# Kernel tuning notes

Measured on AMD Instinct MI355X. Metric: run time of the kernel, lower is better.

The kernel has to match this reference:

```python
import jax, jax.numpy as jnp
import numpy as np

N_HEADS = 16


def setup_inputs() -> dict:
    key = jax.random.key(0)
    k1, k2, k3, k4, k5 = jax.random.split(key, 5)
    B, S, D = 2, 2048, 1024
    return {
        "query": jax.random.normal(k1, (B, S, D), dtype=jnp.float32),
        "key": jax.random.normal(k2, (B, S, D), dtype=jnp.float32),
        "value": jax.random.normal(k3, (B, S, D), dtype=jnp.float32),
        "fc_w": jax.random.normal(k4, (D, D), dtype=jnp.float32) * (1.0 / np.sqrt(D)),
        "fc_b": jax.random.normal(k5, (D,), dtype=jnp.float32) * 0.01,
    }


def reference(query, key, value, fc_w, fc_b):
    b, s, d = query.shape
    head_dim = d // N_HEADS
    q = query.reshape(b, s, N_HEADS, head_dim)
    k = key.reshape(b, s, N_HEADS, head_dim)
    v = value.reshape(b, s, N_HEADS, head_dim)
    # energy: [b, n, q, k]
    energy = jnp.einsum('bqnd,bknd->bnqk', q, k)
    scale = 1.0 / jnp.sqrt(jnp.asarray(head_dim, dtype=energy.dtype))
    attn = jax.nn.softmax(energy * scale, axis=3)
    out = jnp.einsum('bnqk,bknd->bqnd', attn, v).reshape(b, s, d)
    # fc: y = x @ W^T + b (torch Linear convention)
    return out @ fc_w.T + fc_b
```

## Files before the change

kernel.cpp:

```cpp
#include <hip/hip_runtime.h>
#include <hip/hip_bf16.h>

#define BATCH 2
#define SEQ 2048
#define DMODEL 1024
#define NHEADS 16
#define HDIM 64
#define KVBLK 64
#define NCHUNK (SEQ / KVBLK)
#define NITER (NCHUNK / 2)

#define QSCALE 0.180336880f
#define DEFER_THR 8.0f

typedef __bf16 bf16x8 __attribute__((ext_vector_type(8)));
typedef __bf16 bf16x4 __attribute__((ext_vector_type(4)));
typedef float f32x4 __attribute__((ext_vector_type(4)));
typedef float f32x16 __attribute__((ext_vector_type(16)));
typedef unsigned int uint2v __attribute__((ext_vector_type(2)));

union B8u { unsigned int u[4]; bf16x8 v; };

__device__ __forceinline__ unsigned int cvt_pk_bf16(float lo, float hi) {
  unsigned int d;
  asm("v_cvt_pk_bf16_f32 %0, %1, %2" : "=v"(d) : "v"(lo), "v"(hi));
  return d;
}

__device__ __forceinline__ void permlane32_swap(unsigned &a, unsigned &b) {
  auto r = __builtin_amdgcn_permlane32_swap(a, b, false, false);
  unsigned tmp[2];
  __builtin_memcpy(tmp, &r, 8);
  a = tmp[0]; b = tmp[1];
}

__global__ __launch_bounds__(256)
void conv_all(const float* __restrict__ K, __bf16* __restrict__ Kbf,
              const float* __restrict__ V, __bf16* __restrict__ Vt,
              const float* __restrict__ W, __bf16* __restrict__ Wbf) {
  const int p = blockIdx.x;
  __shared__ __bf16 T[64][72];

  if (p < 2048) {
    const int t = p * 256 + threadIdx.x;
    const int d8 = t & 7, key = (t >> 3) & (SEQ - 1), g = t >> 14;
    const float* src = K + ((size_t)(g >> 4) * SEQ + key) * DMODEL +
                       (g & 15) * HDIM + d8 * 8;
    f32x4 a = *reinterpret_cast<const f32x4*>(src);
    f32x4 c = *reinterpret_cast<const f32x4*>(src + 4);
    bf16x8 o;
#pragma unroll
    for (int j = 0; j < 4; ++j) { o[j] = (__bf16)a[j]; o[4 + j] = (__bf16)c[j]; }
    *reinterpret_cast<bf16x8*>(Kbf + (size_t)t * 8) = o;
  } else if (p < 3072) {
    const int blk = p - 2048;
    const int g = blk >> 5, c0 = (blk & 31) * 64;
    const int b = g >> 4, h = g & 15;
    {
      const int key = threadIdx.x >> 2, dq = threadIdx.x & 3;
      const float* src = V + ((size_t)(b * SEQ) + c0 + key) * DMODEL +
                         h * HDIM + dq * 16;
#pragma unroll
      for (int i = 0; i < 4; ++i) {
        f32x4 v = *reinterpret_cast<const f32x4*>(src + 4 * i);
        bf16x4 o;
#pragma unroll
        for (int j = 0; j < 4; ++j) o[j] = (__bf16)v[j];
        *reinterpret_cast<bf16x4*>(&T[key][dq * 16 + 4 * i]) = o;
      }
    }
    __syncthreads();
    {
      const int d = threadIdx.x >> 2, kq = threadIdx.x & 3;
      bf16x8 r0, r1;
#pragma unroll
      for (int i = 0; i < 8; ++i) {
        r0[i] = T[kq * 16 + i][d];
        r1[i] = T[kq * 16 + 8 + i][d];
      }
      __bf16* dst = Vt + ((size_t)g * HDIM + d) * SEQ + c0 + kq * 16;
      *reinterpret_cast<bf16x8*>(dst) = r0;
      *reinterpret_cast<bf16x8*>(dst + 8) = r1;
    }
  } else {
    const int t = (p - 3072) * 256 + threadIdx.x;
    f32x4 a = *reinterpret_cast<const f32x4*>(W + (size_t)t * 8);
    f32x4 c = *reinterpret_cast<const f32x4*>(W + (size_t)t * 8 + 4);
    bf16x8 o;
#pragma unroll
    for (int j = 0; j < 4; ++j) { o[j] = (__bf16)a[j]; o[4 + j] = (__bf16)c[j]; }
    *reinterpret_cast<bf16x8*>(Wbf + (size_t)t * 8) = o;
  }
}

__global__ __launch_bounds__(512, 4)
void attn_kernel(const float* __restrict__ Q, const __bf16* __restrict__ Kbf,
                 const __bf16* __restrict__ Vt, __bf16* __restrict__ O) {
  const int p = blockIdx.x;
  const int xcd = p & 7, slot = p >> 3;
  const int g = xcd + 8 * (slot >> 4);
  const int b = g >> 4, h = g & 15;
  const int q0 = (slot & 15) * 128;

  const int tid = threadIdx.x;
  const int wave = tid >> 6, lane = tid & 63;
  const int qg = wave & 3, ks = wave >> 2;
  const int l31 = lane & 31, hi = lane >> 5;
  const int ob = hi << 4;
  const int swz = (l31 & 7) << 4;

  __shared__ __align__(16) __bf16 SM[2][2][64 * 64];
  __shared__ float mlb[2][4][32];

  const int qrow = q0 + (qg << 5) + l31;
  const float* qp = Q + ((size_t)(b * SEQ + qrow)) * DMODEL + h * HDIM;
  bf16x8 qf[4];
#pragma unroll
  for (int kd = 0; kd < 4; ++kd) {
    f32x4 a = *reinterpret_cast<const f32x4*>(qp + kd * 16 + hi * 8);
    f32x4 c = *reinterpret_cast<const f32x4*>(qp + kd * 16 + hi * 8 + 4);
#pragma unroll
    for (int j = 0; j < 4; ++j) {
      qf[kd][j]     = (__bf16)(a[j] * QSCALE);
      qf[kd][4 + j] = (__bf16)(c[j] * QSCALE);
    }
  }

  f32x16 oacc0, oacc1;
#pragma unroll
  for (int r = 0; r < 16; ++r) { oacc0[r] = 0.f; oacc1[r] = 0.f; }
  float m_run = -1e30f, l_run = 0.f;

  const __bf16* kgb = Kbf + (size_t)g * SEQ * HDIM;
  const __bf16* vgb = Vt + (size_t)g * HDIM * SEQ;

  const int t2 = tid & 255;
  const int sk_key = t2 >> 2, sk_dq = t2 & 3;
  const int sv_dim = t2 >> 2, sv_kq = t2 & 3;
  const int ksw = (sk_key & 7) << 4;
  const int vsw = (sv_dim & 7) << 4;

  bf16x8 kr0, kr1, vr0, vr1;

#define STAGE_LOAD(C0)                                                        \
  do {                                                                        \
    const __bf16* kc = kgb + (size_t)(C0 + sk_key) * HDIM + sk_dq * 16;       \
    kr0 = *reinterpret_cast<const bf16x8*>(kc);                               \
    kr1 = *reinterpret_cast<const bf16x8*>(kc + 8);                           \
    const __bf16* vc = vgb + (size_t)sv_dim * SEQ + (C0) + sv_kq * 16;        \
    vr0 = *reinterpret_cast<const bf16x8*>(vc);                               \
    vr1 = *reinterpret_cast<const bf16x8*>(vc + 8);                           \
  } while (0)

#define STAGE_WRITE()                                                         \
  do {                                                                        \
    char* kdst = (char*)(&SM[ks][0][0]) + sk_key * 128;                       \
    *reinterpret_cast<bf16x8*>(kdst + (((sk_dq << 5)) ^ ksw)) = kr0;          \
    *reinterpret_cast<bf16x8*>(kdst + (((sk_dq << 5) | 16) ^ ksw)) = kr1;     \
    char* vdst = (char*)(&SM[ks][1][0]) + sv_dim * 128;                       \
    *reinterpret_cast<bf16x8*>(vdst + (((sv_kq << 5)) ^ vsw)) = vr0;          \
    *reinterpret_cast<bf16x8*>(vdst + (((sv_kq << 5) | 16) ^ vsw)) = vr1;     \
  } while (0)

  STAGE_LOAD(ks * NITER * KVBLK);
  STAGE_WRITE();
  __syncthreads();
  STAGE_LOAD((ks * NITER + 1) * KVBLK);

  for (int i = 0; i < NITER; ++i) {
    const char* kb = (const char*)(&SM[ks][0][0]);
    const char* vb = (const char*)(&SM[ks][1][0]);

    f32x16 s0, s1;
#pragma unroll
    for (int r = 0; r < 16; ++r) { s0[r] = 0.f; s1[r] = 0.f; }
    __builtin_amdgcn_s_setprio(1);
#pragma unroll
    for (int kd = 0; kd < 4; ++kd) {
      bf16x8 a0 = *reinterpret_cast<const bf16x8*>(
          kb + l31 * 128 + (((kd << 5) | ob) ^ swz));
      bf16x8 a1 = *reinterpret_cast<const bf16x8*>(
          kb + (32 + l31) * 128 + (((kd << 5) | ob) ^ swz));
      s0 = __builtin_amdgcn_mfma_f32_32x32x16_bf16(a0, qf[kd], s0, 0, 0, 0);
      s1 = __builtin_amdgcn_mfma_f32_32x32x16_bf16(a1, qf[kd], s1, 0, 0, 0);
    }
    __builtin_amdgcn_s_setprio(0);

    float m8[8];
#pragma unroll
    for (int r = 0; r < 8; ++r)
      m8[r] = fmaxf(fmaxf(s0[r], s0[r + 8]), fmaxf(s1[r], s1[r + 8]));
    float pm = fmaxf(fmaxf(fmaxf(m8[0], m8[1]), fmaxf(m8[2], m8[3])),
                     fmaxf(fmaxf(m8[4], m8[5]), fmaxf(m8[6], m8[7])));
    pm = fmaxf(pm, __shfl_xor(pm, 32, 64));

    if (!__all(pm <= m_run + DEFER_THR)) {
      float mu = fmaxf(m_run, pm);
      float al = __builtin_amdgcn_exp2f(m_run - mu);
      m_run = mu;
      l_run *= al;
#pragma unroll
      for (int r = 0; r < 16; ++r) { oacc0[r] *= al; oacc1[r] *= al; }
    }

#pragma unroll
    for (int r = 0; r < 16; ++r) {
      s0[r] = __builtin_amdgcn_exp2f(s0[r] - m_run);
      s1[r] = __builtin_amdgcn_exp2f(s1[r] - m_run);
    }
    float t8[8];
#pragma unroll
    for (int r = 0; r < 8; ++r)
      t8[r] = (s0[r] + s0[r + 8]) + (s1[r] + s1[r + 8]);
    float ts = ((t8[0] + t8[1]) + (t8[2] + t8[3])) +
               ((t8[4] + t8[5]) + (t8[6] + t8[7]));
    ts += __shfl_xor(ts, 32, 64);
    l_run += ts;

    B8u pfr[4];
#pragma unroll
    for (int kq = 0; kq < 4; ++kq) {
      f32x16 ps = (kq < 2) ? s0 : s1;
      const int r0 = (kq & 1) * 8;
      unsigned lo0 = cvt_pk_bf16(ps[r0 + 0], ps[r0 + 1]);
      unsigned lo1 = cvt_pk_bf16(ps[r0 + 2], ps[r0 + 3]);
      unsigned h0  = cvt_pk_bf16(ps[r0 + 4], ps[r0 + 5]);
      unsigned h1  = cvt_pk_bf16(ps[r0 + 6], ps[r0 + 7]);
      permlane32_swap(lo0, h0);
      permlane32_swap(lo1, h1);
      pfr[kq].u[0] = lo0; pfr[kq].u[1] = lo1;
      pfr[kq].u[2] = h0;  pfr[kq].u[3] = h1;
    }

    __builtin_amdgcn_s_setprio(1);
#pragma unroll
    for (int kq = 0; kq < 4; ++kq) {
      bf16x8 v0 = *reinterpret_cast<const bf16x8*>(
          vb + l31 * 128 + (((kq << 5) | ob) ^ swz));
      bf16x8 v1 = *reinterpret_cast<const bf16x8*>(
          vb + (32 + l31) * 128 + (((kq << 5) | ob) ^ swz));
      oacc0 = __builtin_amdgcn_mfma_f32_32x32x16_bf16(v0, pfr[kq].v, oacc0, 0, 0, 0);
      oacc1 = __builtin_amdgcn_mfma_f32_32x32x16_bf16(v1, pfr[kq].v, oacc1, 0, 0, 0);
    }
    __builtin_amdgcn_s_setprio(0);

    __syncthreads();
    if (i + 1 < NITER) {
      STAGE_WRITE();
      if (i + 2 < NITER) STAGE_LOAD((ks * NITER + i + 2) * KVBLK);
    }
    __syncthreads();
  }

  float* Ob = (float*)&SM[0][0][0];

  if (ks == 1) {
    if (hi == 0) { mlb[0][qg][l31] = m_run; mlb[1][qg][l31] = l_run; }
#pragma unroll
    for (int dt = 0; dt < 2; ++dt) {
      f32x16 oa = dt ? oacc1 : oacc0;
#pragma unroll
      for (int r = 0; r < 16; ++r) {
        int dim = dt * 32 + (r & 3) + 8 * (r >> 2) + 4 * hi;
        Ob[(qg * 64 + dim) * 32 + l31] = oa[r];
      }
    }
  }
  __syncthreads();

  if (ks == 0) {
    float m1 = mlb[0][qg][l31], l1 = mlb[1][qg][l31];
    float m = fmaxf(m_run, m1);
    float a0 = __builtin_amdgcn_exp2f(m_run - m);
    float a1 = __builtin_amdgcn_exp2f(m1 - m);
    const float inv = 1.0f / (a0 * l_run + a1 * l1);
    __bf16* op = O + ((size_t)(b * SEQ + qrow)) * DMODEL + h * HDIM;
#pragma unroll
    for (int dt = 0; dt < 2; ++dt) {
      f32x16 oa = dt ? oacc1 : oacc0;
#pragma unroll
      for (int a = 0; a < 4; ++a) {
        float e[4];
#pragma unroll
        for (int j = 0; j < 4; ++j) {
          int r = 4 * a + j;
          int dim = dt * 32 + (r & 3) + 8 * (r >> 2) + 4 * hi;
          float opart = Ob[(qg * 64 + dim) * 32 + l31];
          e[j] = (oa[r] * a0 + opart * a1) * inv;
        }
        uint2v w;
        w[0] = cvt_pk_bf16(e[0], e[1]);
        w[1] = cvt_pk_bf16(e[2], e[3]);
        *reinterpret_cast<uint2v*>((char*)op + (dt * 32 + a * 8 + hi * 4) * 2) = w;
      }
    }
  }
#undef STAGE_LOAD
#undef STAGE_WRITE
}

__global__ __launch_bounds__(256)
void fc_kernel(const __bf16* __restrict__ X, const __bf16* __restrict__ W,
               const float* __restrict__ bias, float* __restrict__ Y) {
  const int p = blockIdx.x;
  const int xcd = p & 7, slot = p >> 3;
  const int m0 = (xcd + 8 * (slot >> 4)) * 128;
  const int n0 = (slot & 15) * 64;

  const int tid = threadIdx.x;
  const int wave = tid >> 6, lane = tid & 63;
  const int g = lane >> 4, lr = lane & 15;
  const int wm = wave >> 1, wn = wave & 1;

  __shared__ __bf16 As[128][72];
  __shared__ __bf16 Bs[64][72];

  f32x4 acc[4][2];
#pragma unroll
  for (int i = 0; i < 4; ++i)
#pragma unroll
    for (int j = 0; j < 2; ++j) acc[i][j] = (f32x4){0.f, 0.f, 0.f, 0.f};

  float bv[2];
#pragma unroll
  for (int j = 0; j < 2; ++j) bv[j] = bias[n0 + wn * 32 + 16 * j + lr];

  bf16x8 av[4], wv[2];

#define FC_LOAD(KK)                                                          \
  do {                                                                       \
    _Pragma("unroll") for (int e = 0; e < 4; ++e) {                          \
      int idx = tid + 256 * e;                                               \
      int row = idx >> 3, k8 = idx & 7;                                      \
      av[e] = *reinterpret_cast<const bf16x8*>(                              \
          X + (size_t)(m0 + row) * DMODEL + (KK) + k8 * 8);                  \
    }                                                                        \
    _Pragma("unroll") for (int e = 0; e < 2; ++e) {                          \
      int idx = tid + 256 * e;                                               \
      int row = idx >> 3, k8 = idx & 7;                                      \
      wv[e] = *reinterpret_cast<const bf16x8*>(                              \
          W + (size_t)(n0 + row) * DMODEL + (KK) + k8 * 8);                  \
    }                                                                        \
  } while (0)

#define FC_WRITE()                                                           \
  do {                                                                       \
    _Pragma("unroll") for (int e = 0; e < 4; ++e) {                          \
      int idx = tid + 256 * e;                                               \
      int row = idx >> 3, k8 = idx & 7;                                      \
      *reinterpret_cast<bf16x8*>(&As[row][k8 * 8]) = av[e];                  \
    }                                                                        \
    _Pragma("unroll") for (int e = 0; e < 2; ++e) {                          \
      int idx = tid + 256 * e;                                               \
      int row = idx >> 3, k8 = idx & 7;                                      \
      *reinterpret_cast<bf16x8*>(&Bs[row][k8 * 8]) = wv[e];                  \
    }                                                                        \
  } while (0)

  FC_LOAD(0);

  for (int kk = 0; kk < DMODEL; kk += 64) {
    __syncthreads();
    FC_WRITE();
    __syncthreads();
    if (kk + 64 < DMODEL) FC_LOAD(kk + 64);

#pragma unroll
    for (int ks2 = 0; ks2 < 2; ++ks2) {
      bf16x8 af[4], bfr[2];
#pragma unroll
      for (int i = 0; i < 4; ++i)
        af[i] = *reinterpret_cast<const bf16x8*>(
            &As[wm * 64 + 16 * i + lr][ks2 * 32 + g * 8]);
#pragma unroll
      for (int j = 0; j < 2; ++j)
        bfr[j] = *reinterpret_cast<const bf16x8*>(
            &Bs[wn * 32 + 16 * j + lr][ks2 * 32 + g * 8]);
#pragma unroll
      for (int i = 0; i < 4; ++i)
#pragma unroll
        for (int j = 0; j < 2; ++j)
          acc[i][j] = __builtin_amdgcn_mfma_f32_16x16x32_bf16(
              af[i], bfr[j], acc[i][j], 0, 0, 0);
    }
  }

#pragma unroll
  for (int i = 0; i < 4; ++i) {
    int m = m0 + wm * 64 + 16 * i + g * 4;
#pragma unroll
    for (int j = 0; j < 2; ++j) {
      int n = n0 + wn * 32 + 16 * j + lr;
      float* yp = Y + (size_t)m * DMODEL + n;
#pragma unroll
      for (int r = 0; r < 4; ++r) yp[(size_t)r * DMODEL] = acc[i][j][r] + bv[j];
    }
  }
#undef FC_LOAD
#undef FC_WRITE
}

extern "C" void kernel_launch(void* const* d_in, const int* in_sizes, int n_in,
                              void* d_out, int out_size, void* d_ws, size_t ws_size,
                              hipStream_t stream) {
  const float* q    = (const float*)d_in[0];
  const float* k    = (const float*)d_in[1];
  const float* v    = (const float*)d_in[2];
  const float* w    = (const float*)d_in[3];
  const float* bias = (const float*)d_in[4];
  float* out = (float*)d_out;

  char* ws = (char*)d_ws;
  __bf16* O   = (__bf16*)(ws);
  __bf16* Kbf = (__bf16*)(ws + (8u << 20));
  __bf16* Vt  = (__bf16*)(ws + (16u << 20));
  __bf16* Wbf = (__bf16*)(ws + (24u << 20));

  conv_all<<<dim3(3584), 256, 0, stream>>>(k, Kbf, v, Vt, w, Wbf);
  attn_kernel<<<dim3(512), 512, 0, stream>>>(q, Kbf, Vt, O);
  fc_kernel<<<dim3(512), 256, 0, stream>>>(O, Wbf, bias, out);
}
```

Before: 83.82 us.

## Split KV four ways per block with 64-row query tiles and tree combine

Each attention block now covers 64 query rows instead of 128, and its eight waves split the sequence into four KV partitions instead of two. The grid doubles to 1024 blocks and the KV chunk shrinks from 64 to 32 keys. The V tile drops its XOR swizzle for a padded row stride. Partial softmax states are merged in stages through shared memory, with three dump/combine rounds. The aim is better load balance and occupancy across CUs, at the cost of more barriers per key processed, smaller MFMA batches per iteration and extra combine work.

```diff
diff --git a/kernel.cpp b/kernel.cpp
--- a/kernel.cpp
+++ b/kernel.cpp
@@ -6,9 +6,9 @@
 #define DMODEL 1024
 #define NHEADS 16
 #define HDIM 64
-#define KVBLK 64
-#define NCHUNK (SEQ / KVBLK)
-#define NITER (NCHUNK / 2)
+#define NSPLIT 4
+#define KVB 32
+#define NIT (SEQ / NSPLIT / KVB)
 
 #define QSCALE 0.180336880f
 #define DEFER_THR 8.0f
@@ -98,19 +98,20 @@
                  const __bf16* __restrict__ Vt, __bf16* __restrict__ O) {
   const int p = blockIdx.x;
   const int xcd = p & 7, slot = p >> 3;
-  const int g = xcd + 8 * (slot >> 4);
+  const int g = xcd + 8 * (slot >> 5);
   const int b = g >> 4, h = g & 15;
-  const int q0 = (slot & 15) * 128;
+  const int q0 = (slot & 31) * 64;
 
   const int tid = threadIdx.x;
   const int wave = tid >> 6, lane = tid & 63;
-  const int qg = wave & 3, ks = wave >> 2;
+  const int qg = wave & 1, ks = wave >> 1;
   const int l31 = lane & 31, hi = lane >> 5;
   const int ob = hi << 4;
   const int swz = (l31 & 7) << 4;
 
-  __shared__ __align__(16) __bf16 SM[2][2][64 * 64];
-  __shared__ float mlb[2][4][32];
+  __shared__ __align__(16) __bf16 SK[4][32 * 64];
+  __shared__ __align__(16) __bf16 SV[4][64 * 40];
+  __shared__ float mlb[3][2][2][32];
 
   const int qrow = q0 + (qg << 5) + l31;
   const float* qp = Q + ((size_t)(b * SEQ + qrow)) * DMODEL + h * HDIM;
@@ -134,62 +135,57 @@
   const __bf16* kgb = Kbf + (size_t)g * SEQ * HDIM;
   const __bf16* vgb = Vt + (size_t)g * HDIM * SEQ;
 
-  const int t2 = tid & 255;
+  const int t2 = tid & 127;
   const int sk_key = t2 >> 2, sk_dq = t2 & 3;
-  const int sv_dim = t2 >> 2, sv_kq = t2 & 3;
+  const int sv_dim = t2 >> 1, sv_kh = t2 & 1;
   const int ksw = (sk_key & 7) << 4;
-  const int vsw = (sv_dim & 7) << 4;
 
   bf16x8 kr0, kr1, vr0, vr1;
 
 #define STAGE_LOAD(C0)                                                        \
   do {                                                                        \
-    const __bf16* kc = kgb + (size_t)(C0 + sk_key) * HDIM + sk_dq * 16;       \
+    const __bf16* kc = kgb + (size_t)((C0) + sk_key) * HDIM + sk_dq * 16;     \
     kr0 = *reinterpret_cast<const bf16x8*>(kc);                               \
     kr1 = *reinterpret_cast<const bf16x8*>(kc + 8);                           \
-    const __bf16* vc = vgb + (size_t)sv_dim * SEQ + (C0) + sv_kq * 16;        \
+    const __bf16* vc = vgb + (size_t)sv_dim * SEQ + (C0) + sv_kh * 16;        \
     vr0 = *reinterpret_cast<const bf16x8*>(vc);                               \
     vr1 = *reinterpret_cast<const bf16x8*>(vc + 8);                           \
   } while (0)
 
 #define STAGE_WRITE()                                                         \
   do {                                                                        \
-    char* kdst = (char*)(&SM[ks][0][0]) + sk_key * 128;                       \
+    char* kdst = (char*)(&SK[ks][0]) + sk_key * 128;                          \
     *reinterpret_cast<bf16x8*>(kdst + (((sk_dq << 5)) ^ ksw)) = kr0;          \
     *reinterpret_cast<bf16x8*>(kdst + (((sk_dq << 5) | 16) ^ ksw)) = kr1;     \
-    char* vdst = (char*)(&SM[ks][1][0]) + sv_dim * 128;                       \
-    *reinterpret_cast<bf16x8*>(vdst + (((sv_kq << 5)) ^ vsw)) = vr0;          \
-    *reinterpret_cast<bf16x8*>(vdst + (((sv_kq << 5) | 16) ^ vsw)) = vr1;     \
-  } while (0)
-
-  STAGE_LOAD(ks * NITER * KVBLK);
+    char* vdst = (char*)(&SV[ks][0]) + sv_dim * 80 + sv_kh * 32;              \
+    *reinterpret_cast<bf16x8*>(vdst) = vr0;                                   \
+    *reinterpret_cast<bf16x8*>(vdst + 16) = vr1;                              \
+  } while (0)
+
+  STAGE_LOAD(ks * 512);
   STAGE_WRITE();
   __syncthreads();
-  STAGE_LOAD((ks * NITER + 1) * KVBLK);
-
-  for (int i = 0; i < NITER; ++i) {
-    const char* kb = (const char*)(&SM[ks][0][0]);
-    const char* vb = (const char*)(&SM[ks][1][0]);
-
-    f32x16 s0, s1;
-#pragma unroll
-    for (int r = 0; r < 16; ++r) { s0[r] = 0.f; s1[r] = 0.f; }
+  STAGE_LOAD(ks * 512 + KVB);
+
+  for (int i = 0; i < NIT; ++i) {
+    const char* kb = (const char*)(&SK[ks][0]);
+    const char* vb = (const char*)(&SV[ks][0]);
+
+    f32x16 s;
+#pragma unroll
+    for (int r = 0; r < 16; ++r) s[r] = 0.f;
     __builtin_amdgcn_s_setprio(1);
 #pragma unroll
     for (int kd = 0; kd < 4; ++kd) {
       bf16x8 a0 = *reinterpret_cast<const bf16x8*>(
           kb + l31 * 128 + (((kd << 5) | ob) ^ swz));
-      bf16x8 a1 = *reinterpret_cast<const bf16x8*>(
-          kb + (32 + l31) * 128 + (((kd << 5) | ob) ^ swz));
-      s0 = __builtin_amdgcn_mfma_f32_32x32x16_bf16(a0, qf[kd], s0, 0, 0, 0);
-      s1 = __builtin_amdgcn_mfma_f32_32x32x16_bf16(a1, qf[kd], s1, 0, 0, 0);
+      s = __builtin_amdgcn_mfma_f32_32x32x16_bf16(a0, qf[kd], s, 0, 0, 0);
     }
     __builtin_amdgcn_s_setprio(0);
 
     float m8[8];
 #pragma unroll
-    for (int r = 0; r < 8; ++r)
-      m8[r] = fmaxf(fmaxf(s0[r], s0[r + 8]), fmaxf(s1[r], s1[r + 8]));
+    for (int r = 0; r < 8; ++r) m8[r] = fmaxf(s[r], s[r + 8]);
     float pm = fmaxf(fmaxf(fmaxf(m8[0], m8[1]), fmaxf(m8[2], m8[3])),
                      fmaxf(fmaxf(m8[4], m8[5]), fmaxf(m8[6], m8[7])));
     pm = fmaxf(pm, __shfl_xor(pm, 32, 64));
@@ -204,28 +200,23 @@
     }
 
 #pragma unroll
-    for (int r = 0; r < 16; ++r) {
-      s0[r] = __builtin_amdgcn_exp2f(s0[r] - m_run);
-      s1[r] = __builtin_amdgcn_exp2f(s1[r] - m_run);
-    }
+    for (int r = 0; r < 16; ++r) s[r] = __builtin_amdgcn_exp2f(s[r] - m_run);
     float t8[8];
 #pragma unroll
-    for (int r = 0; r < 8; ++r)
-      t8[r] = (s0[r] + s0[r + 8]) + (s1[r] + s1[r + 8]);
+    for (int r = 0; r < 8; ++r) t8[r] = s[r] + s[r + 8];
     float ts = ((t8[0] + t8[1]) + (t8[2] + t8[3])) +
                ((t8[4] + t8[5]) + (t8[6] + t8[7]));
     ts += __shfl_xor(ts, 32, 64);
     l_run += ts;
 
-    B8u pfr[4];
-#pragma unroll
-    for (int kq = 0; kq < 4; ++kq) {
-      f32x16 ps = (kq < 2) ? s0 : s1;
-      const int r0 = (kq & 1) * 8;
-      unsigned lo0 = cvt_pk_bf16(ps[r0 + 0], ps[r0 + 1]);
-      unsigned lo1 = cvt_pk_bf16(ps[r0 + 2], ps[r0 + 3]);
-      unsigned h0  = cvt_pk_bf16(ps[r0 + 4], ps[r0 + 5]);
-      unsigned h1  = cvt_pk_bf16(ps[r0 + 6], ps[r0 + 7]);
+    B8u pfr[2];
+#pragma unroll
+    for (int kq = 0; kq < 2; ++kq) {
+      const int r0 = kq * 8;
+      unsigned lo0 = cvt_pk_bf16(s[r0 + 0], s[r0 + 1]);
+      unsigned lo1 = cvt_pk_bf16(s[r0 + 2], s[r0 + 3]);
+      unsigned h0  = cvt_pk_bf16(s[r0 + 4], s[r0 + 5]);
+      unsigned h1  = cvt_pk_bf16(s[r0 + 6], s[r0 + 7]);
       permlane32_swap(lo0, h0);
       permlane32_swap(lo1, h1);
       pfr[kq].u[0] = lo0; pfr[kq].u[1] = lo1;
@@ -234,69 +225,85 @@
 
     __builtin_amdgcn_s_setprio(1);
 #pragma unroll
-    for (int kq = 0; kq < 4; ++kq) {
+    for (int kq = 0; kq < 2; ++kq) {
       bf16x8 v0 = *reinterpret_cast<const bf16x8*>(
-          vb + l31 * 128 + (((kq << 5) | ob) ^ swz));
+          vb + l31 * 80 + ((kq << 5) | ob));
       bf16x8 v1 = *reinterpret_cast<const bf16x8*>(
-          vb + (32 + l31) * 128 + (((kq << 5) | ob) ^ swz));
+          vb + (32 + l31) * 80 + ((kq << 5) | ob));
       oacc0 = __builtin_amdgcn_mfma_f32_32x32x16_bf16(v0, pfr[kq].v, oacc0, 0, 0, 0);
       oacc1 = __builtin_amdgcn_mfma_f32_32x32x16_bf16(v1, pfr[kq].v, oacc1, 0, 0, 0);
     }
     __builtin_amdgcn_s_setprio(0);
 
     __syncthreads();
-    if (i + 1 < NITER) {
+    if (i + 1 < NIT) {
       STAGE_WRITE();
-      if (i + 2 < NITER) STAGE_LOAD((ks * NITER + i + 2) * KVBLK);
+      if (i + 2 < NIT) STAGE_LOAD(ks * 512 + (i + 2) * KVB);
     }
     __syncthreads();
   }
 
-  float* Ob = (float*)&SM[0][0][0];
-
-  if (ks == 1) {
-    if (hi == 0) { mlb[0][qg][l31] = m_run; mlb[1][qg][l31] = l_run; }
+  float* ObA = (float*)&SK[0][0];
+  float* ObB = (float*)&SV[0][0];
+
+#define DUMP(OB, MI)                                                          \
+  do {                                                                        \
+    if (hi == 0) { mlb[MI][0][qg][l31] = m_run; mlb[MI][1][qg][l31] = l_run; }\
+    _Pragma("unroll") for (int dt = 0; dt < 2; ++dt) {                        \
+      f32x16 oa = dt ? oacc1 : oacc0;                                         \
+      _Pragma("unroll") for (int r = 0; r < 16; ++r) {                        \
+        int dim = dt * 32 + (r & 3) + 8 * (r >> 2) + 4 * hi;                  \
+        (OB)[((qg << 6) + dim) * 32 + l31] = oa[r];                           \
+      }                                                                       \
+    }                                                                         \
+  } while (0)
+
+#define COMBINE(OB, MI)                                                       \
+  do {                                                                        \
+    float m1 = mlb[MI][0][qg][l31], l1 = mlb[MI][1][qg][l31];                 \
+    float mm = fmaxf(m_run, m1);                                              \
+    float a0 = __builtin_amdgcn_exp2f(m_run - mm);                            \
+    float a1 = __builtin_amdgcn_exp2f(m1 - mm);                               \
+    _Pragma("unroll") for (int dt = 0; dt < 2; ++dt) {                        \
+      _Pragma("unroll") for (int r = 0; r < 16; ++r) {                        \
+        int dim = dt * 32 + (r & 3) + 8 * (r >> 2) + 4 * hi;                  \
+        float opart = (OB)[((qg << 6) + dim) * 32 + l31];                     \
+        if (dt) oacc1[r] = oacc1[r] * a0 + opart * a1;                        \
+        else    oacc0[r] = oacc0[r] * a0 + opart * a1;                        \
+      }                                                                       \
+    }                                                                         \
+    l_run = l_run * a0 + l1 * a1;                                             \
+    m_run = mm;                                                               \
+  } while (0)
+
+  if (ks == 1) DUMP(ObA, 0);
+  if (ks == 2) DUMP(ObB, 1);
+  __syncthreads();
+  if (ks == 0) { COMBINE(ObA, 0); COMBINE(ObB, 1); }
+  __syncthreads();
+  if (ks == 3) DUMP(ObA, 2);
+  __syncthreads();
+
+  if (ks == 0) {
+    COMBINE(ObA, 2);
+    const float inv = 1.0f / l_run;
+    __bf16* op = O + ((size_t)(b * SEQ + qrow)) * DMODEL + h * HDIM;
 #pragma unroll
     for (int dt = 0; dt < 2; ++dt) {
       f32x16 oa = dt ? oacc1 : oacc0;
 #pragma unroll
-      for (int r = 0; r < 16; ++r) {
-        int dim = dt * 32 + (r & 3) + 8 * (r >> 2) + 4 * hi;
-        Ob[(qg * 64 + dim) * 32 + l31] = oa[r];
-      }
-    }
-  }
-  __syncthreads();
-
-  if (ks == 0) {
-    float m1 = mlb[0][qg][l31], l1 = mlb[1][qg][l31];
-    float m = fmaxf(m_run, m1);
-    float a0 = __builtin_amdgcn_exp2f(m_run - m);
-    float a1 = __builtin_amdgcn_exp2f(m1 - m);
-    const float inv = 1.0f / (a0 * l_run + a1 * l1);
-    __bf16* op = O + ((size_t)(b * SEQ + qrow)) * DMODEL + h * HDIM;
-#pragma unroll
-    for (int dt = 0; dt < 2; ++dt) {
-      f32x16 oa = dt ? oacc1 : oacc0;
-#pragma unroll
       for (int a = 0; a < 4; ++a) {
-        float e[4];
-#pragma unroll
-        for (int j = 0; j < 4; ++j) {
-          int r = 4 * a + j;
-          int dim = dt * 32 + (r & 3) + 8 * (r >> 2) + 4 * hi;
-          float opart = Ob[(qg * 64 + dim) * 32 + l31];
-          e[j] = (oa[r] * a0 + opart * a1) * inv;
-        }
         uint2v w;
-        w[0] = cvt_pk_bf16(e[0], e[1]);
-        w[1] = cvt_pk_bf16(e[2], e[3]);
+        w[0] = cvt_pk_bf16(oa[4 * a + 0] * inv, oa[4 * a + 1] * inv);
+        w[1] = cvt_pk_bf16(oa[4 * a + 2] * inv, oa[4 * a + 3] * inv);
         *reinterpret_cast<uint2v*>((char*)op + (dt * 32 + a * 8 + hi * 4) * 2) = w;
       }
     }
   }
 #undef STAGE_LOAD
 #undef STAGE_WRITE
+#undef DUMP
+#undef COMBINE
 }
 
 __global__ __launch_bounds__(256)
@@ -417,6 +424,6 @@
   __bf16* Wbf = (__bf16*)(ws + (24u << 20));
 
   conv_all<<<dim3(3584), 256, 0, stream>>>(k, Kbf, v, Vt, w, Wbf);
-  attn_kernel<<<dim3(512), 512, 0, stream>>>(q, Kbf, Vt, O);
+  attn_kernel<<<dim3(1024), 512, 0, stream>>>(q, Kbf, Vt, O);
   fc_kernel<<<dim3(512), 256, 0, stream>>>(O, Wbf, bias, out);
 }
```

After: 95.59 us. 1.14x slower.
